# Kernel tuning notes

Measured on AMD Instinct MI355X. Metric: run time of the kernel, lower is better.

Reference implementation:

```python
import jax, jax.numpy as jnp
import numpy as np


def position_encoding(feature_size, d_model):
    pos = jnp.arange(feature_size, dtype=jnp.float32)[:, None]
    _2i = jnp.arange(0, d_model, 2, dtype=jnp.float32)
    ang = pos / jnp.power(10000.0, _2i / d_model)  # [F, D/2]
    pe = jnp.zeros((feature_size, d_model), dtype=jnp.float32)
    pe = pe.at[:, 0::2].set(jnp.sin(ang))
    pe = pe.at[:, 1::2].set(jnp.cos(ang))
    return pe


def setup_inputs() -> dict:
    key = jax.random.key(0)
    ks = jax.random.split(key, 11)
    B, F, D, T, V = 32, 512, 256, 32, 128
    sc = 0.02
    return {
        "f": jax.random.normal(ks[0], (B, F, D), dtype=jnp.float32),
        "decoder_input_ids": jax.random.randint(ks[1], (B, T), 0, V),
        "emb": sc * jax.random.normal(ks[2], (V, D), dtype=jnp.float32),
        "w_e": sc * jax.random.normal(ks[3], (D, D), dtype=jnp.float32),
        "w_h": sc * jax.random.normal(ks[4], (D, D), dtype=jnp.float32),
        "w_f": sc * jax.random.normal(ks[5], (D, D), dtype=jnp.float32),
        "w_q": sc * jax.random.normal(ks[6], (D, D), dtype=jnp.float32),
        "w_s": sc * jax.random.normal(ks[7], (D, D), dtype=jnp.float32),
        "w_g": sc * jax.random.normal(ks[8], (D, 2 * D), dtype=jnp.float32),
        "w_ih": sc * jax.random.normal(ks[9], (4 * D, 2 * D), dtype=jnp.float32),
        "w_hh": sc * jax.random.normal(ks[10], (4 * D, D), dtype=jnp.float32),
    }


def reference(f, decoder_input_ids, emb, w_e, w_h, w_f, w_q, w_s, w_g, w_ih, w_hh):
    B, F, D = f.shape
    q = position_encoding(F, D)                      # [F, D]
    dec = emb[decoder_input_ids]                     # [B, T, D]
    # loop-invariant attention terms, hoisted: w_f(f) + w_q(q)
    base = jnp.einsum('bfd,od->bfo', f, w_f) + (q @ w_q.T)[None]  # [B, F, D]
    fq = f + q[None]                                 # [B, F, D]

    def step(carry, x_t):
        h, cell, s, cp = carry
        # LSTMCell (bias=False), torch gate order i, f, g, o
        xin = jnp.concatenate([x_t, cp], axis=-1)    # [B, 2D]
        gates = xin @ w_ih.T + h @ w_hh.T            # [B, 4D]
        gi, gf, gg, go = jnp.split(gates, 4, axis=-1)
        cell = jax.nn.sigmoid(gf) * cell + jax.nn.sigmoid(gi) * jnp.tanh(gg)
        h = jax.nn.sigmoid(go) * jnp.tanh(cell)
        # Bahdanau-style energy; softmax over feature (last) dim per source
        t_in = jnp.tanh((h @ w_h.T)[:, None] + base + jnp.einsum('bfd,od->bfo', s, w_s))
        e = jnp.einsum('bfd,od->bfo', t_in, w_e)     # [B, F, D]
        alpha = jax.nn.softmax(e, axis=-1)
        s = s + alpha
        c = (alpha * f).sum(1)                       # [B, D]
        cp = (alpha * fq).sum(1)                     # [B, D]
        pred = jnp.concatenate([c, h], axis=-1) @ w_g.T  # [B, D]
        return (h, cell, s, cp), pred

    z = jnp.zeros((B, D), dtype=f.dtype)
    carry0 = (z, z, jnp.zeros_like(f), z)
    _, preds = jax.lax.scan(step, carry0, jnp.swapaxes(dec, 0, 1))  # [T, B, D]
    return jnp.swapaxes(preds, 0, 1)                 # [B, T, D]
```

## Files before the change

### kernel.cpp

```cpp
#include <hip/hip_runtime.h>
#include <math.h>

#define NB 32
#define NF 512
#define ND 256
#define NT 32
#define RPB 32
#define NTILE (NF / RPB)
#define XS 260

typedef __attribute__((ext_vector_type(8))) short bf16x8;
typedef __attribute__((ext_vector_type(4))) short bf16x4;
typedef __attribute__((ext_vector_type(4))) float f32x4;

__device__ __forceinline__ float sigmoidf_(float x) { return 1.0f / (1.0f + __expf(-x)); }

__device__ __forceinline__ short f2bf(float x) {
    union { float f; unsigned u; } v; v.f = x;
    unsigned r = (v.u + 0x7FFF + ((v.u >> 16) & 1)) >> 16;
    return (short)r;
}

__global__ void pe_kernel(float* __restrict__ q) {
    int p = blockIdx.x;
    int d = threadIdx.x;
    float i2 = (float)((d >> 1) << 1);
    float rate = expf(-9.210340371976184f * (i2 / (float)ND));
    float ang = (float)p * rate;
    q[p * ND + d] = (d & 1) ? cosf(ang) : sinf(ang);
}

__global__ void wcvt_kernel(const float* __restrict__ w, short* __restrict__ wb, int n) {
    int i = blockIdx.x * 256 + threadIdx.x;
    if (i < n) wb[i] = f2bf(w[i]);
}

__global__ void wprep_kernel(const float* __restrict__ w_h, const float* __restrict__ w_g,
                             float* __restrict__ w_hT, float* __restrict__ w_gT) {
    int k = blockIdx.x;
    int o = threadIdx.x;
    if (k < ND) w_hT[(size_t)k * ND + o] = w_h[(size_t)o * ND + k];
    w_gT[(size_t)k * ND + o] = w_g[(size_t)o * 512 + k];
}

__global__ void qwq_kernel(const float* __restrict__ q, const float* __restrict__ w_q,
                           float* __restrict__ qwq) {
    int p = blockIdx.x;
    int o = threadIdx.x;
    __shared__ float qs[ND];
    qs[o] = q[(size_t)p * ND + o];
    __syncthreads();
    const float4* wr = (const float4*)(w_q + (size_t)o * ND);
    float acc = 0.f;
    for (int k4 = 0; k4 < ND / 4; ++k4) {
        float4 w = wr[k4];
        int k = 4 * k4;
        acc += qs[k] * w.x + qs[k + 1] * w.y + qs[k + 2] * w.z + qs[k + 3] * w.w;
    }
    qwq[(size_t)p * ND + o] = acc;
}

__global__ void base_kernel(const float* __restrict__ fin, const float* __restrict__ w_f,
                            const float* __restrict__ qwq, float* __restrict__ bsum) {
    int b = blockIdx.x / NTILE;
    int f0 = (blockIdx.x % NTILE) * RPB;
    int o = threadIdx.x;
    __shared__ float fs[RPB][ND];
    #pragma unroll
    for (int r = 0; r < RPB; ++r)
        fs[r][o] = fin[((size_t)(b * NF + f0 + r)) * ND + o];
    __syncthreads();
    float acc[RPB];
    #pragma unroll
    for (int r = 0; r < RPB; ++r) acc[r] = 0.f;
    const float4* wr = (const float4*)(w_f + (size_t)o * ND);
    for (int k4 = 0; k4 < ND / 4; ++k4) {
        float4 w = wr[k4];
        int k = 4 * k4;
        #pragma unroll
        for (int r = 0; r < RPB; ++r)
            acc[r] += fs[r][k] * w.x + fs[r][k + 1] * w.y + fs[r][k + 2] * w.z + fs[r][k + 3] * w.w;
    }
    #pragma unroll
    for (int r = 0; r < RPB; ++r)
        bsum[((size_t)(b * NF + f0 + r)) * ND + o] = acc[r] + qwq[(size_t)(f0 + r) * ND + o];
}

#define ZSTRIDE 769
__global__ void gates_kernel(int t, int mode,
                             const int* __restrict__ ids, const float* __restrict__ emb,
                             const float* __restrict__ cpart, const float* __restrict__ cppart,
                             const float* __restrict__ h,
                             const float* __restrict__ w_ih, const float* __restrict__ w_hh,
                             const float* __restrict__ w_gT,
                             float* __restrict__ gatesT, float* __restrict__ out) {
    extern __shared__ float lds[];
    int bid = blockIdx.x;
    int tid = threadIdx.x;

    if (bid < 128) {
        if (!(mode & 1)) return;
        int j0 = bid * 8;
        float* wl = lds;
        float* zl = lds + 8 * 768;
        float4* wl4 = (float4*)wl;
        for (int cc = 0; cc < 6; ++cc) {
            int idx4 = tid + cc * 256;
            int flat = idx4 * 4;
            int r = flat / 768;
            int col = flat - r * 768;
            float4 v;
            if (col < 512) v = *(const float4*)(w_ih + (size_t)(j0 + r) * 512 + col);
            else           v = *(const float4*)(w_hh + (size_t)(j0 + r) * 256 + (col - 512));
            wl4[idx4] = v;
        }
        for (int b = 0; b < NB; ++b) {
            int d = tid;
            float xv = (t < NT) ? emb[(size_t)ids[b * NT + t] * ND + d] : 0.f;
            float cpsum = 0.f;
            if (t > 0) {
                #pragma unroll
                for (int tl = 0; tl < NTILE; ++tl)
                    cpsum += cppart[((size_t)tl * NB + b) * ND + d];
            }
            float hv = h[(size_t)b * ND + d];
            zl[b * ZSTRIDE + d]       = xv;
            zl[b * ZSTRIDE + 256 + d] = cpsum;
            zl[b * ZSTRIDE + 512 + d] = hv;
        }
        __syncthreads();
        int r = tid >> 5;
        int b = tid & 31;
        const float4* wr4 = (const float4*)(wl + r * 768);
        const float* zb = zl + b * ZSTRIDE;
        float acc = 0.f;
        #pragma unroll 8
        for (int k4 = 0; k4 < 192; ++k4) {
            float4 w = wr4[k4];
            int k = 4 * k4;
            acc += w.x * zb[k] + w.y * zb[k + 1] + w.z * zb[k + 2] + w.w * zb[k + 3];
        }
        gatesT[(size_t)b * 1024 + (j0 + r)] = acc;
    } else {
        if (!(mode & 2)) return;
        int b = bid - 128;
        float* zp = lds;
        float csum = 0.f;
        #pragma unroll
        for (int tl = 0; tl < NTILE; ++tl)
            csum += cpart[((size_t)tl * NB + b) * ND + tid];
        zp[tid] = csum;
        zp[256 + tid] = h[(size_t)b * ND + tid];
        __syncthreads();
        float p = 0.f;
        #pragma unroll 8
        for (int k = 0; k < 512; ++k)
            p += zp[k] * w_gT[(size_t)k * ND + tid];
        out[((size_t)b * NT + (t - 1)) * ND + tid] = p;
    }
}

__global__ void __launch_bounds__(256, 2) attn_step_kernel(
        float* __restrict__ bsum,
        const float* __restrict__ fin, const float* __restrict__ qpe,
        const float* __restrict__ gatesT,
        const float* __restrict__ cell_prev, float* __restrict__ cell_next,
        float* __restrict__ h_next,
        const float* __restrict__ w_hT,
        const short* __restrict__ w_e_bf, const short* __restrict__ w_s_bf,
        float* __restrict__ cpart, float* __restrict__ cppart) {
    int b = blockIdx.x / NTILE;
    int tile = blockIdx.x % NTILE;
    int f0 = tile * RPB;
    int tid = threadIdx.x;
    int l = tid & 63;
    int wv = tid >> 6;
    int c15 = l & 15;
    int g = l >> 4;
    int c = l;
    int o0 = wv * 64;

    __shared__ __align__(16) short tin_bf[RPB * ND];
    __shared__ float xfer[RPB * XS];
    __shared__ float cred[2][1024];
    __shared__ float sred[RPB][5];
    char* tb = (char*)tin_bf;
    float* hn = xfer;
    float* hwhl = xfer + 256;

    {
        float gi = gatesT[(size_t)b * 1024 + tid];
        float gf = gatesT[(size_t)b * 1024 + 256 + tid];
        float gg = gatesT[(size_t)b * 1024 + 512 + tid];
        float go = gatesT[(size_t)b * 1024 + 768 + tid];
        float cold = cell_prev[(size_t)b * ND + tid];
        float cnew = sigmoidf_(gf) * cold + sigmoidf_(gi) * tanhf(gg);
        float hval = sigmoidf_(go) * tanhf(cnew);
        if (tile == 0) {
            cell_next[(size_t)b * ND + tid] = cnew;
            h_next[(size_t)b * ND + tid] = hval;
        }
        hn[tid] = hval;
    }
    __syncthreads();
    {
        float a = 0.f;
        #pragma unroll 8
        for (int k = 0; k < ND; ++k)
            a += hn[k] * w_hT[(size_t)k * ND + tid];
        hwhl[tid] = a;
    }
    __syncthreads();

    float4 bsv4[8];
    {
        float4 hwh4 = *(const float4*)&hwhl[4 * c];
        #pragma unroll
        for (int i = 0; i < 8; ++i) {
            int r = wv + 4 * i;
            bsv4[i] = *(const float4*)(bsum + ((size_t)(b * NF + f0 + r)) * ND + 4 * c);
            bf16x4 tv;
            tv.x = f2bf(tanhf(hwh4.x + bsv4[i].x));
            tv.y = f2bf(tanhf(hwh4.y + bsv4[i].y));
            tv.z = f2bf(tanhf(hwh4.z + bsv4[i].z));
            tv.w = f2bf(tanhf(hwh4.w + bsv4[i].w));
            *(bf16x4*)(tb + ((r * 512 + 8 * c) ^ ((r & 7) << 4))) = tv;
        }
    }
    __syncthreads();

    f32x4 acc[2][4];
    #pragma unroll
    for (int mt = 0; mt < 2; ++mt)
        #pragma unroll
        for (int nt = 0; nt < 4; ++nt)
            acc[mt][nt] = (f32x4)0.f;
    #pragma unroll
    for (int ks = 0; ks < 8; ++ks) {
        int kb = ks * 32 + g * 8;
        bf16x8 afr[2];
        #pragma unroll
        for (int mt = 0; mt < 2; ++mt) {
            int row = mt * 16 + c15;
            afr[mt] = *(const bf16x8*)(tb + ((row * 512 + kb * 2) ^ ((row & 7) << 4)));
        }
        #pragma unroll
        for (int nt = 0; nt < 4; ++nt) {
            int o = o0 + nt * 16 + c15;
            bf16x8 bfr = *(const bf16x8*)(w_e_bf + (size_t)o * ND + kb);
            #pragma unroll
            for (int mt = 0; mt < 2; ++mt)
                acc[mt][nt] = __builtin_amdgcn_mfma_f32_16x16x32_bf16(afr[mt], bfr, acc[mt][nt], 0, 0, 0);
        }
    }

    {
        float ps[2][4];
        #pragma unroll
        for (int mt = 0; mt < 2; ++mt)
            #pragma unroll
            for (int reg = 0; reg < 4; ++reg) ps[mt][reg] = 0.f;
        #pragma unroll
        for (int mt = 0; mt < 2; ++mt)
            #pragma unroll
            for (int nt = 0; nt < 4; ++nt)
                #pragma unroll
                for (int reg = 0; reg < 4; ++reg) {
                    float a = __expf(acc[mt][nt][reg]);
                    acc[mt][nt][reg] = a;
                    ps[mt][reg] += a;
                }
        #pragma unroll
        for (int off = 1; off <= 8; off <<= 1)
            #pragma unroll
            for (int mt = 0; mt < 2; ++mt)
                #pragma unroll
                for (int reg = 0; reg < 4; ++reg)
                    ps[mt][reg] += __shfl_xor(ps[mt][reg], off);
        if (c15 == 0) {
            #pragma unroll
            for (int mt = 0; mt < 2; ++mt)
                #pragma unroll
                for (int reg = 0; reg < 4; ++reg)
                    sred[mt * 16 + g * 4 + reg][wv] = ps[mt][reg];
        }
        __syncthreads();
        #pragma unroll
        for (int mt = 0; mt < 2; ++mt)
            #pragma unroll
            for (int reg = 0; reg < 4; ++reg) {
                int r = mt * 16 + g * 4 + reg;
                float inv = 1.0f / (sred[r][0] + sred[r][1] + sred[r][2] + sred[r][3]);
                #pragma unroll
                for (int nt = 0; nt < 4; ++nt)
                    acc[mt][nt][reg] *= inv;
            }
    }

    #pragma unroll
    for (int mt = 0; mt < 2; ++mt)
        #pragma unroll
        for (int reg = 0; reg < 4; ++reg) {
            int r = mt * 16 + g * 4 + reg;
            #pragma unroll
            for (int nt = 0; nt < 4; ++nt)
                xfer[r * XS + o0 + nt * 16 + c15] = acc[mt][nt][reg];
        }
    __syncthreads();

    {
        float4 pc4 = {0.f, 0.f, 0.f, 0.f}, pcp4 = {0.f, 0.f, 0.f, 0.f};
        #pragma unroll
        for (int i = 0; i < 8; ++i) {
            int r = wv + 4 * i;
            float4 a4 = *(const float4*)&xfer[r * XS + 4 * c];
            float4 f4 = *(const float4*)(fin + ((size_t)(b * NF + f0 + r)) * ND + 4 * c);
            float4 q4 = *(const float4*)(qpe + ((size_t)(f0 + r)) * ND + 4 * c);
            pc4.x += a4.x * f4.x;  pcp4.x += a4.x * (f4.x + q4.x);
            pc4.y += a4.y * f4.y;  pcp4.y += a4.y * (f4.y + q4.y);
            pc4.z += a4.z * f4.z;  pcp4.z += a4.z * (f4.z + q4.z);
            pc4.w += a4.w * f4.w;  pcp4.w += a4.w * (f4.w + q4.w);
            bf16x4 av;
            av.x = f2bf(a4.x); av.y = f2bf(a4.y); av.z = f2bf(a4.z); av.w = f2bf(a4.w);
            *(bf16x4*)(tb + ((r * 512 + 8 * c) ^ ((r & 7) << 4))) = av;
        }
        *(float4*)&cred[0][wv * 256 + 4 * c] = pc4;
        *(float4*)&cred[1][wv * 256 + 4 * c] = pcp4;
    }
    __syncthreads();

    {
        float pc  = cred[0][tid] + cred[0][256 + tid] + cred[0][512 + tid] + cred[0][768 + tid];
        float pcp = cred[1][tid] + cred[1][256 + tid] + cred[1][512 + tid] + cred[1][768 + tid];
        cpart [((size_t)tile * NB + b) * ND + tid] = pc;
        cppart[((size_t)tile * NB + b) * ND + tid] = pcp;
    }

    {
        f32x4 acc2[2][4];
        #pragma unroll
        for (int mt = 0; mt < 2; ++mt)
            #pragma unroll
            for (int nt = 0; nt < 4; ++nt)
                acc2[mt][nt] = (f32x4)0.f;
        #pragma unroll
        for (int ks = 0; ks < 8; ++ks) {
            int kb = ks * 32 + g * 8;
            bf16x8 afr[2];
            #pragma unroll
            for (int mt = 0; mt < 2; ++mt) {
                int row = mt * 16 + c15;
                afr[mt] = *(const bf16x8*)(tb + ((row * 512 + kb * 2) ^ ((row & 7) << 4)));
            }
            #pragma unroll
            for (int nt = 0; nt < 4; ++nt) {
                int o = o0 + nt * 16 + c15;
                bf16x8 bfr = *(const bf16x8*)(w_s_bf + (size_t)o * ND + kb);
                #pragma unroll
                for (int mt = 0; mt < 2; ++mt)
                    acc2[mt][nt] = __builtin_amdgcn_mfma_f32_16x16x32_bf16(afr[mt], bfr, acc2[mt][nt], 0, 0, 0);
            }
        }
        __syncthreads();
        #pragma unroll
        for (int mt = 0; mt < 2; ++mt)
            #pragma unroll
            for (int reg = 0; reg < 4; ++reg) {
                int r = mt * 16 + g * 4 + reg;
                #pragma unroll
                for (int nt = 0; nt < 4; ++nt)
                    xfer[r * XS + o0 + nt * 16 + c15] = acc2[mt][nt][reg];
            }
    }
    __syncthreads();

    #pragma unroll
    for (int i = 0; i < 8; ++i) {
        int r = wv + 4 * i;
        float4 x4 = *(const float4*)&xfer[r * XS + 4 * c];
        float4 o4;
        o4.x = bsv4[i].x + x4.x;
        o4.y = bsv4[i].y + x4.y;
        o4.z = bsv4[i].z + x4.z;
        o4.w = bsv4[i].w + x4.w;
        *(float4*)(bsum + ((size_t)(b * NF + f0 + r)) * ND + 4 * c) = o4;
    }
}

extern "C" void kernel_launch(void* const* d_in, const int* in_sizes, int n_in,
                              void* d_out, int out_size, void* d_ws, size_t ws_size,
                              hipStream_t stream) {
    const float* fin  = (const float*)d_in[0];
    const int*   ids  = (const int*)  d_in[1];
    const float* emb  = (const float*)d_in[2];
    const float* w_e  = (const float*)d_in[3];
    const float* w_h  = (const float*)d_in[4];
    const float* w_f  = (const float*)d_in[5];
    const float* w_q  = (const float*)d_in[6];
    const float* w_s  = (const float*)d_in[7];
    const float* w_g  = (const float*)d_in[8];
    const float* w_ih = (const float*)d_in[9];
    const float* w_hh = (const float*)d_in[10];
    float* out = (float*)d_out;
    float* ws  = (float*)d_ws;

    size_t off = 0;
    float* q      = ws + off; off += (size_t)NF * ND;
    float* qwq    = ws + off; off += (size_t)NF * ND;
    float* bsum   = ws + off; off += (size_t)NB * NF * ND;
    float* h0     = ws + off; off += (size_t)NB * ND;
    float* h1     = ws + off; off += (size_t)NB * ND;
    float* cell0  = ws + off; off += (size_t)NB * ND;
    float* cell1  = ws + off; off += (size_t)NB * ND;
    float* gatesT = ws + off; off += (size_t)NB * 1024;
    float* cpart  = ws + off; off += (size_t)NTILE * NB * ND;
    float* cppart = ws + off; off += (size_t)NTILE * NB * ND;
    float* w_hT   = ws + off; off += (size_t)ND * ND;
    float* w_gT   = ws + off; off += (size_t)512 * ND;
    short* w_e_bf = (short*)(ws + off); off += (size_t)ND * ND / 2;
    short* w_s_bf = (short*)(ws + off); off += (size_t)ND * ND / 2;

    float* hbuf[2]    = { h0, h1 };
    float* cellbuf[2] = { cell0, cell1 };

    hipMemsetAsync(h0, 0, sizeof(float) * NB * ND, stream);
    hipMemsetAsync(cell0, 0, sizeof(float) * NB * ND, stream);

    pe_kernel<<<NF, ND, 0, stream>>>(q);
    wcvt_kernel<<<ND * ND / 256, 256, 0, stream>>>(w_e, w_e_bf, ND * ND);
    wcvt_kernel<<<ND * ND / 256, 256, 0, stream>>>(w_s, w_s_bf, ND * ND);
    wprep_kernel<<<512, ND, 0, stream>>>(w_h, w_g, w_hT, w_gT);
    qwq_kernel<<<NF, ND, 0, stream>>>(q, w_q, qwq);
    base_kernel<<<NB * NTILE, ND, 0, stream>>>(fin, w_f, qwq, bsum);

    const size_t gates_lds = (size_t)(8 * 768 + NB * ZSTRIDE) * sizeof(float);

    for (int t = 0; t < NT; ++t) {
        int mode = (t > 0) ? 3 : 1;
        int p = t & 1;
        gates_kernel<<<160, ND, gates_lds, stream>>>(t, mode, ids, emb, cpart, cppart, hbuf[p],
                                                     w_ih, w_hh, w_gT, gatesT, out);
        attn_step_kernel<<<NB * NTILE, ND, 0, stream>>>(bsum, fin, q, gatesT,
                                                        cellbuf[p], cellbuf[p ^ 1], hbuf[p ^ 1],
                                                        w_hT, w_e_bf, w_s_bf, cpart, cppart);
    }
    gates_kernel<<<160, ND, gates_lds, stream>>>(NT, 2, ids, emb, cpart, cppart, hbuf[0],
                                                 w_ih, w_hh, w_gT, gatesT, out);
}
```

Before: 2.680 ms.

## Store bsum and f/q in MFMA fragment layout, drop LDS transpose staging

Stores the running attention sum bsum in a per-thread MFMA-fragment-ordered layout so each thread reads and writes its accumulator slice directly, with no LDS transpose buffer. Adds a prep kernel that converts f and the positional encoding to bf16 in the same fragment layout, which halves their per-step read traffic, and computes the c/cp partial sums in registers with cross-lane shuffles. The smaller LDS footprint lets launch bounds rise to 3 blocks per CU. In exchange, f and q are held at bf16 precision in the context sums, and the tanh input writes to LDS become scalar 2-byte stores.

```diff
diff --git a/kernel.cpp b/kernel.cpp
--- a/kernel.cpp
+++ b/kernel.cpp
@@ -7,7 +7,7 @@
 #define NT 32
 #define RPB 32
 #define NTILE (NF / RPB)
-#define XS 260
+#define NBLK (NB * NTILE)
 
 typedef __attribute__((ext_vector_type(8))) short bf16x8;
 typedef __attribute__((ext_vector_type(4))) short bf16x4;
@@ -19,6 +19,11 @@
     union { float f; unsigned u; } v; v.f = x;
     unsigned r = (v.u + 0x7FFF + ((v.u >> 16) & 1)) >> 16;
     return (short)r;
+}
+__device__ __forceinline__ float bf2f(short s) {
+    union { unsigned u; float f; } v;
+    v.u = ((unsigned)(unsigned short)s) << 16;
+    return v.f;
 }
 
 __global__ void pe_kernel(float* __restrict__ q) {
@@ -61,9 +66,10 @@
 }
 
 __global__ void base_kernel(const float* __restrict__ fin, const float* __restrict__ w_f,
-                            const float* __restrict__ qwq, float* __restrict__ bsum) {
-    int b = blockIdx.x / NTILE;
-    int f0 = (blockIdx.x % NTILE) * RPB;
+                            const float* __restrict__ qwq, float* __restrict__ bsum_cl) {
+    int blk = blockIdx.x;
+    int b = blk / NTILE;
+    int f0 = (blk % NTILE) * RPB;
     int o = threadIdx.x;
     __shared__ float fs[RPB][ND];
     #pragma unroll
@@ -82,8 +88,34 @@
             acc[r] += fs[r][k] * w.x + fs[r][k + 1] * w.y + fs[r][k + 2] * w.z + fs[r][k + 3] * w.w;
     }
     #pragma unroll
-    for (int r = 0; r < RPB; ++r)
-        bsum[((size_t)(b * NF + f0 + r)) * ND + o] = acc[r] + qwq[(size_t)(f0 + r) * ND + o];
+    for (int r = 0; r < RPB; ++r) {
+        int owner = (o & 0xC0) + (r & 12) * 4 + (o & 15);
+        int j = (r >> 4) * 16 + ((o >> 4) & 3) * 4 + (r & 3);
+        bsum_cl[(size_t)blk * 8192 + owner * 32 + j] = acc[r] + qwq[(size_t)(f0 + r) * ND + o];
+    }
+}
+
+__global__ void clprep_kernel(const float* __restrict__ fin, const float* __restrict__ qpe,
+                              short* __restrict__ fin_cl, short* __restrict__ q_cl) {
+    int blk = blockIdx.x;
+    int b = blk >> 4;
+    int tile = blk & 15;
+    int f0 = tile * RPB;
+    int tid = threadIdx.x;
+    int g = (tid & 63) >> 4;
+    int c15 = tid & 15;
+    int o0 = tid & 0xC0;
+    #pragma unroll
+    for (int j = 0; j < 32; ++j) {
+        int mt = j >> 4, nt = (j >> 2) & 3, reg = j & 3;
+        int r = mt * 16 + g * 4 + reg;
+        int col = o0 + nt * 16 + c15;
+        fin_cl[(size_t)blk * 8192 + tid * 32 + j] =
+            f2bf(fin[((size_t)(b * NF + f0 + r)) * ND + col]);
+        if (b == 0)
+            q_cl[(size_t)tile * 8192 + tid * 32 + j] =
+                f2bf(qpe[(size_t)(f0 + r) * ND + col]);
+    }
 }
 
 #define ZSTRIDE 769
@@ -160,33 +192,29 @@
     }
 }
 
-__global__ void __launch_bounds__(256, 2) attn_step_kernel(
-        float* __restrict__ bsum,
-        const float* __restrict__ fin, const float* __restrict__ qpe,
+__global__ void __launch_bounds__(256, 3) attn_step_kernel(
+        float* __restrict__ bsum_cl,
+        const short* __restrict__ fin_cl, const short* __restrict__ q_cl,
         const float* __restrict__ gatesT,
         const float* __restrict__ cell_prev, float* __restrict__ cell_next,
         float* __restrict__ h_next,
         const float* __restrict__ w_hT,
         const short* __restrict__ w_e_bf, const short* __restrict__ w_s_bf,
         float* __restrict__ cpart, float* __restrict__ cppart) {
-    int b = blockIdx.x / NTILE;
-    int tile = blockIdx.x % NTILE;
-    int f0 = tile * RPB;
+    int blk = blockIdx.x;
+    int b = blk / NTILE;
+    int tile = blk % NTILE;
     int tid = threadIdx.x;
     int l = tid & 63;
-    int wv = tid >> 6;
     int c15 = l & 15;
     int g = l >> 4;
-    int c = l;
-    int o0 = wv * 64;
+    int o0 = tid & 0xC0;
 
     __shared__ __align__(16) short tin_bf[RPB * ND];
-    __shared__ float xfer[RPB * XS];
-    __shared__ float cred[2][1024];
+    __shared__ float hn[ND];
+    __shared__ float hwhl[ND];
     __shared__ float sred[RPB][5];
     char* tb = (char*)tin_bf;
-    float* hn = xfer;
-    float* hwhl = xfer + 256;
 
     {
         float gi = gatesT[(size_t)b * 1024 + tid];
@@ -212,20 +240,27 @@
     }
     __syncthreads();
 
-    float4 bsv4[8];
-    {
-        float4 hwh4 = *(const float4*)&hwhl[4 * c];
-        #pragma unroll
-        for (int i = 0; i < 8; ++i) {
-            int r = wv + 4 * i;
-            bsv4[i] = *(const float4*)(bsum + ((size_t)(b * NF + f0 + r)) * ND + 4 * c);
-            bf16x4 tv;
-            tv.x = f2bf(tanhf(hwh4.x + bsv4[i].x));
-            tv.y = f2bf(tanhf(hwh4.y + bsv4[i].y));
-            tv.z = f2bf(tanhf(hwh4.z + bsv4[i].z));
-            tv.w = f2bf(tanhf(hwh4.w + bsv4[i].w));
-            *(bf16x4*)(tb + ((r * 512 + 8 * c) ^ ((r & 7) << 4))) = tv;
-        }
+    f32x4 bsv[2][4];
+    {
+        float hw4[4];
+        #pragma unroll
+        for (int nt = 0; nt < 4; ++nt)
+            hw4[nt] = hwhl[o0 + nt * 16 + c15];
+        const f32x4* bsp = (const f32x4*)(bsum_cl + (size_t)blk * 8192 + tid * 32);
+        #pragma unroll
+        for (int mt = 0; mt < 2; ++mt)
+            #pragma unroll
+            for (int nt = 0; nt < 4; ++nt) {
+                f32x4 bv = bsp[mt * 4 + nt];
+                bsv[mt][nt] = bv;
+                int col = o0 + nt * 16 + c15;
+                #pragma unroll
+                for (int reg = 0; reg < 4; ++reg) {
+                    int r = mt * 16 + g * 4 + reg;
+                    float tv = tanhf(hw4[nt] + bv[reg]);
+                    *(short*)(tb + ((r * 512 + col * 2) ^ ((r & 7) << 4))) = f2bf(tv);
+                }
+            }
     }
     __syncthreads();
 
@@ -282,7 +317,7 @@
             for (int mt = 0; mt < 2; ++mt)
                 #pragma unroll
                 for (int reg = 0; reg < 4; ++reg)
-                    sred[mt * 16 + g * 4 + reg][wv] = ps[mt][reg];
+                    sred[mt * 16 + g * 4 + reg][tid >> 6] = ps[mt][reg];
         }
         __syncthreads();
         #pragma unroll
@@ -303,38 +338,56 @@
         for (int reg = 0; reg < 4; ++reg) {
             int r = mt * 16 + g * 4 + reg;
             #pragma unroll
+            for (int nt = 0; nt < 4; ++nt) {
+                int col = o0 + nt * 16 + c15;
+                *(short*)(tb + ((r * 512 + col * 2) ^ ((r & 7) << 4))) = f2bf(acc[mt][nt][reg]);
+            }
+        }
+
+    {
+        const bf16x8* fp = (const bf16x8*)(fin_cl + (size_t)blk * 8192 + tid * 32);
+        const bf16x8* qp = (const bf16x8*)(q_cl + (size_t)tile * 8192 + tid * 32);
+        short fb[32], qb[32];
+        #pragma unroll
+        for (int i8 = 0; i8 < 4; ++i8) {
+            bf16x8 fv8 = fp[i8];
+            bf16x8 qv8 = qp[i8];
+            #pragma unroll
+            for (int sl = 0; sl < 8; ++sl) { fb[i8 * 8 + sl] = fv8[sl]; qb[i8 * 8 + sl] = qv8[sl]; }
+        }
+        float pc[4], pcp[4];
+        #pragma unroll
+        for (int nt = 0; nt < 4; ++nt) { pc[nt] = 0.f; pcp[nt] = 0.f; }
+        #pragma unroll
+        for (int mt = 0; mt < 2; ++mt)
+            #pragma unroll
             for (int nt = 0; nt < 4; ++nt)
-                xfer[r * XS + o0 + nt * 16 + c15] = acc[mt][nt][reg];
-        }
-    __syncthreads();
-
-    {
-        float4 pc4 = {0.f, 0.f, 0.f, 0.f}, pcp4 = {0.f, 0.f, 0.f, 0.f};
-        #pragma unroll
-        for (int i = 0; i < 8; ++i) {
-            int r = wv + 4 * i;
-            float4 a4 = *(const float4*)&xfer[r * XS + 4 * c];
-            float4 f4 = *(const float4*)(fin + ((size_t)(b * NF + f0 + r)) * ND + 4 * c);
-            float4 q4 = *(const float4*)(qpe + ((size_t)(f0 + r)) * ND + 4 * c);
-            pc4.x += a4.x * f4.x;  pcp4.x += a4.x * (f4.x + q4.x);
-            pc4.y += a4.y * f4.y;  pcp4.y += a4.y * (f4.y + q4.y);
-            pc4.z += a4.z * f4.z;  pcp4.z += a4.z * (f4.z + q4.z);
-            pc4.w += a4.w * f4.w;  pcp4.w += a4.w * (f4.w + q4.w);
-            bf16x4 av;
-            av.x = f2bf(a4.x); av.y = f2bf(a4.y); av.z = f2bf(a4.z); av.w = f2bf(a4.w);
-            *(bf16x4*)(tb + ((r * 512 + 8 * c) ^ ((r & 7) << 4))) = av;
-        }
-        *(float4*)&cred[0][wv * 256 + 4 * c] = pc4;
-        *(float4*)&cred[1][wv * 256 + 4 * c] = pcp4;
-    }
-    __syncthreads();
-
-    {
-        float pc  = cred[0][tid] + cred[0][256 + tid] + cred[0][512 + tid] + cred[0][768 + tid];
-        float pcp = cred[1][tid] + cred[1][256 + tid] + cred[1][512 + tid] + cred[1][768 + tid];
-        cpart [((size_t)tile * NB + b) * ND + tid] = pc;
-        cppart[((size_t)tile * NB + b) * ND + tid] = pcp;
-    }
+                #pragma unroll
+                for (int reg = 0; reg < 4; ++reg) {
+                    int j = mt * 16 + nt * 4 + reg;
+                    float a = acc[mt][nt][reg];
+                    float fv = bf2f(fb[j]);
+                    float qv = bf2f(qb[j]);
+                    pc[nt] += a * fv;
+                    pcp[nt] += a * (fv + qv);
+                }
+        #pragma unroll
+        for (int off = 16; off <= 32; off <<= 1)
+            #pragma unroll
+            for (int nt = 0; nt < 4; ++nt) {
+                pc[nt]  += __shfl_xor(pc[nt], off);
+                pcp[nt] += __shfl_xor(pcp[nt], off);
+            }
+        if (g == 0) {
+            #pragma unroll
+            for (int nt = 0; nt < 4; ++nt) {
+                int col = o0 + nt * 16 + c15;
+                cpart [((size_t)tile * NB + b) * ND + col] = pc[nt];
+                cppart[((size_t)tile * NB + b) * ND + col] = pcp[nt];
+            }
+        }
+    }
+    __syncthreads();
 
     {
         f32x4 acc2[2][4];
@@ -361,29 +414,15 @@
                     acc2[mt][nt] = __builtin_amdgcn_mfma_f32_16x16x32_bf16(afr[mt], bfr, acc2[mt][nt], 0, 0, 0);
             }
         }
-        __syncthreads();
-        #pragma unroll
-        for (int mt = 0; mt < 2; ++mt)
-            #pragma unroll
-            for (int reg = 0; reg < 4; ++reg) {
-                int r = mt * 16 + g * 4 + reg;
-                #pragma unroll
-                for (int nt = 0; nt < 4; ++nt)
-                    xfer[r * XS + o0 + nt * 16 + c15] = acc2[mt][nt][reg];
-            }
-    }
-    __syncthreads();
-
-    #pragma unroll
-    for (int i = 0; i < 8; ++i) {
-        int r = wv + 4 * i;
-        float4 x4 = *(const float4*)&xfer[r * XS + 4 * c];
-        float4 o4;
-        o4.x = bsv4[i].x + x4.x;
-        o4.y = bsv4[i].y + x4.y;
-        o4.z = bsv4[i].z + x4.z;
-        o4.w = bsv4[i].w + x4.w;
-        *(float4*)(bsum + ((size_t)(b * NF + f0 + r)) * ND + 4 * c) = o4;
+        f32x4* bsp = (f32x4*)(bsum_cl + (size_t)blk * 8192 + tid * 32);
+        #pragma unroll
+        for (int mt = 0; mt < 2; ++mt)
+            #pragma unroll
+            for (int nt = 0; nt < 4; ++nt) {
+                f32x4 v = bsv[mt][nt];
+                v += acc2[mt][nt];
+                bsp[mt * 4 + nt] = v;
+            }
     }
 }
 
@@ -405,20 +444,22 @@
     float* ws  = (float*)d_ws;
 
     size_t off = 0;
-    float* q      = ws + off; off += (size_t)NF * ND;
-    float* qwq    = ws + off; off += (size_t)NF * ND;
-    float* bsum   = ws + off; off += (size_t)NB * NF * ND;
-    float* h0     = ws + off; off += (size_t)NB * ND;
-    float* h1     = ws + off; off += (size_t)NB * ND;
-    float* cell0  = ws + off; off += (size_t)NB * ND;
-    float* cell1  = ws + off; off += (size_t)NB * ND;
-    float* gatesT = ws + off; off += (size_t)NB * 1024;
-    float* cpart  = ws + off; off += (size_t)NTILE * NB * ND;
-    float* cppart = ws + off; off += (size_t)NTILE * NB * ND;
-    float* w_hT   = ws + off; off += (size_t)ND * ND;
-    float* w_gT   = ws + off; off += (size_t)512 * ND;
-    short* w_e_bf = (short*)(ws + off); off += (size_t)ND * ND / 2;
-    short* w_s_bf = (short*)(ws + off); off += (size_t)ND * ND / 2;
+    float* q       = ws + off; off += (size_t)NF * ND;
+    float* qwq     = ws + off; off += (size_t)NF * ND;
+    float* bsum_cl = ws + off; off += (size_t)NB * NF * ND;
+    float* h0      = ws + off; off += (size_t)NB * ND;
+    float* h1      = ws + off; off += (size_t)NB * ND;
+    float* cell0   = ws + off; off += (size_t)NB * ND;
+    float* cell1   = ws + off; off += (size_t)NB * ND;
+    float* gatesT  = ws + off; off += (size_t)NB * 1024;
+    float* cpart   = ws + off; off += (size_t)NTILE * NB * ND;
+    float* cppart  = ws + off; off += (size_t)NTILE * NB * ND;
+    float* w_hT    = ws + off; off += (size_t)ND * ND;
+    float* w_gT    = ws + off; off += (size_t)512 * ND;
+    short* w_e_bf  = (short*)(ws + off); off += (size_t)ND * ND / 2;
+    short* w_s_bf  = (short*)(ws + off); off += (size_t)ND * ND / 2;
+    short* fin_cl  = (short*)(ws + off); off += (size_t)NB * NF * ND / 2;
+    short* q_cl    = (short*)(ws + off); off += (size_t)NF * ND / 2;
 
     float* hbuf[2]    = { h0, h1 };
     float* cellbuf[2] = { cell0, cell1 };
@@ -431,7 +472,8 @@
     wcvt_kernel<<<ND * ND / 256, 256, 0, stream>>>(w_s, w_s_bf, ND * ND);
     wprep_kernel<<<512, ND, 0, stream>>>(w_h, w_g, w_hT, w_gT);
     qwq_kernel<<<NF, ND, 0, stream>>>(q, w_q, qwq);
-    base_kernel<<<NB * NTILE, ND, 0, stream>>>(fin, w_f, qwq, bsum);
+    base_kernel<<<NBLK, ND, 0, stream>>>(fin, w_f, qwq, bsum_cl);
+    clprep_kernel<<<NBLK, ND, 0, stream>>>(fin, q, fin_cl, q_cl);
 
     const size_t gates_lds = (size_t)(8 * 768 + NB * ZSTRIDE) * sizeof(float);
 
@@ -440,9 +482,9 @@
         int p = t & 1;
         gates_kernel<<<160, ND, gates_lds, stream>>>(t, mode, ids, emb, cpart, cppart, hbuf[p],
                                                      w_ih, w_hh, w_gT, gatesT, out);
-        attn_step_kernel<<<NB * NTILE, ND, 0, stream>>>(bsum, fin, q, gatesT,
-                                                        cellbuf[p], cellbuf[p ^ 1], hbuf[p ^ 1],
-                                                        w_hT, w_e_bf, w_s_bf, cpart, cppart);
+        attn_step_kernel<<<NBLK, ND, 0, stream>>>(bsum_cl, fin_cl, q_cl, gatesT,
+                                                  cellbuf[p], cellbuf[p ^ 1], hbuf[p ^ 1],
+                                                  w_hT, w_e_bf, w_s_bf, cpart, cppart);
     }
     gates_kernel<<<160, ND, gates_lds, stream>>>(NT, 2, ids, emb, cpart, cppart, hbuf[0],
                                                  w_ih, w_hh, w_gT, gatesT, out);
```

Measured after the change: 2.912 ms. +8.7%, slower.
